# Performance work log

Measured on AMD Instinct MI355X. Metric: run time of the kernel, lower is better.

Reference implementation:

```python
import jax, jax.numpy as jnp
import numpy as np
from jax import lax

EPS = 1e-5

def conv2d(x, w, pad, dil):
    # x: NCHW, w: OIHW
    return lax.conv_general_dilated(
        x, w, window_strides=(1, 1), padding=[(pad, pad), (pad, pad)],
        rhs_dilation=(dil, dil), dimension_numbers=("NCHW", "OIHW", "NCHW"))

def batchnorm(x, gamma, beta):
    # training-mode BN: batch statistics over (N, H, W), biased variance
    m = x.mean(axis=(0, 2, 3), keepdims=True)
    v = x.var(axis=(0, 2, 3), keepdims=True)
    xh = (x - m) * lax.rsqrt(v + EPS)
    return gamma[None, :, None, None] * xh + beta[None, :, None, None]

def maxpool2(x):
    return lax.reduce_window(x, -jnp.inf, lax.max, (1, 1, 2, 2), (1, 1, 2, 2), "VALID")

def mhsa(x, wq, bq, wk, bk, wv, bv, rel_h, rel_w, heads=1):
    B, C, H, W = x.shape
    N = H * W
    d = C // heads
    q = (conv2d(x, wq, 0, 1) + bq[None, :, None, None]).reshape(B, heads, d, N)
    k = (conv2d(x, wk, 0, 1) + bk[None, :, None, None]).reshape(B, heads, d, N)
    v = (conv2d(x, wv, 0, 1) + bv[None, :, None, None]).reshape(B, heads, d, N)
    # content-content: q^T k -> [B, h, N, N]
    cc = jnp.einsum("bhdn,bhdm->bhnm", q, k)
    # content-position: (rel_h + rel_w) reshaped to [h, d, N], transposed, times q
    pos = (rel_h + rel_w).reshape(heads, d, N)  # broadcast-sum [1,h,d,1,H]+[1,h,d,W,1]
    cp = jnp.einsum("hnd,bhdm->bhnm", jnp.swapaxes(pos, 1, 2), q)
    attn = jax.nn.softmax(cc + cp, axis=-1)
    # out = v @ attn^T
    out = jnp.einsum("bhdn,bhmn->bhdm", v, attn)
    return out.reshape(B, C, H, W)


def setup_inputs() -> dict:
    key = jax.random.key(0)
    ks = jax.random.split(key, 16)
    B, in_ch, out_ch, S = 4, 128, 256, 64
    c4 = out_ch // 4  # 64 = MHSA channel dim
    w_scale = 0.05
    inp = {
        "x": jax.random.normal(ks[0], (B, in_ch, 2 * S, 2 * S), jnp.float32),
        "dc_w1": jax.random.normal(ks[1], (out_ch, in_ch, 3, 3), jnp.float32) * w_scale,
        "dc_b1": jnp.zeros((out_ch,), jnp.float32),
        "dc_g1": jnp.ones((out_ch,), jnp.float32),
        "dc_be1": jnp.zeros((out_ch,), jnp.float32),
        "dc_w2": jax.random.normal(ks[2], (out_ch, out_ch, 3, 3), jnp.float32) * w_scale,
        "dc_b2": jnp.zeros((out_ch,), jnp.float32),
        "dc_g2": jnp.ones((out_ch,), jnp.float32),
        "dc_be2": jnp.zeros((out_ch,), jnp.float32),
        "aspp1_w": jax.random.normal(ks[3], (c4, out_ch, 1, 1), jnp.float32) * w_scale,
        "aspp1_g": jnp.ones((c4,), jnp.float32),
        "aspp1_b": jnp.zeros((c4,), jnp.float32),
        "aspp2_w": jax.random.normal(ks[4], (c4, out_ch, 3, 3), jnp.float32) * w_scale,
        "aspp2_g": jnp.ones((c4,), jnp.float32),
        "aspp2_b": jnp.zeros((c4,), jnp.float32),
        "aspp3_w": jax.random.normal(ks[5], (c4, out_ch, 3, 3), jnp.float32) * w_scale,
        "aspp3_g": jnp.ones((c4,), jnp.float32),
        "aspp3_b": jnp.zeros((c4,), jnp.float32),
        "aspp4_w": jax.random.normal(ks[6], (c4, out_ch, 3, 3), jnp.float32) * w_scale,
        "aspp4_g": jnp.ones((c4,), jnp.float32),
        "aspp4_b": jnp.zeros((c4,), jnp.float32),
        "wq": jax.random.normal(ks[7], (c4, c4, 1, 1), jnp.float32) * w_scale,
        "bq": jnp.zeros((c4,), jnp.float32),
        "wk": jax.random.normal(ks[8], (c4, c4, 1, 1), jnp.float32) * w_scale,
        "bk": jnp.zeros((c4,), jnp.float32),
        "wv": jax.random.normal(ks[9], (c4, c4, 1, 1), jnp.float32) * w_scale,
        "bv": jnp.zeros((c4,), jnp.float32),
        "rel_h": jax.random.normal(ks[10], (1, 1, c4, 1, S), jnp.float32),
        "rel_w": jax.random.normal(ks[11], (1, 1, c4, S, 1), jnp.float32),
    }
    return inp


def reference(x, dc_w1, dc_b1, dc_g1, dc_be1, dc_w2, dc_b2, dc_g2, dc_be2,
              aspp1_w, aspp1_g, aspp1_b, aspp2_w, aspp2_g, aspp2_b,
              aspp3_w, aspp3_g, aspp3_b, aspp4_w, aspp4_g, aspp4_b,
              wq, bq, wk, bk, wv, bv, rel_h, rel_w):
    dilations = (1, 3, 6, 9)
    # mpconv: MaxPool2d(2) -> double_conv
    h = maxpool2(x)
    h = jax.nn.relu(batchnorm(conv2d(h, dc_w1, 1, 1) + dc_b1[None, :, None, None], dc_g1, dc_be1))
    h = jax.nn.relu(batchnorm(conv2d(h, dc_w2, 1, 1) + dc_b2[None, :, None, None], dc_g2, dc_be2))

    aspp = [(aspp1_w, aspp1_g, aspp1_b), (aspp2_w, aspp2_g, aspp2_b),
            (aspp3_w, aspp3_g, aspp3_b), (aspp4_w, aspp4_g, aspp4_b)]
    outs = []
    for (w, g, b), dil in zip(aspp, dilations):
        pad = 0 if dil == 1 else dil
        branch = jax.nn.relu(batchnorm(conv2d(h, w, pad, dil), g, b))
        outs.append(mhsa(branch, wq, bq, wk, bk, wv, bv, rel_h, rel_w))
    return jnp.concatenate(outs, axis=1)
```

## Files before the change

kernel.cpp:

```cpp
#include <hip/hip_runtime.h>
#include <math.h>

constexpr int Bn = 4;
constexpr int S  = 64;
constexpr int N  = 4096;

#define DEV static __device__ __forceinline__

typedef __attribute__((ext_vector_type(8))) short bf16x8;
typedef __attribute__((ext_vector_type(4))) float f32x4;

DEV unsigned short bfc(float x) {
  unsigned u = __float_as_uint(x);
  unsigned r = (u + 0x7FFFu + ((u >> 16) & 1u)) >> 16;
  return (unsigned short)r;
}

DEV void fma4(float4& a, float s, const float4 u) {
  a.x = fmaf(s, u.x, a.x); a.y = fmaf(s, u.y, a.y);
  a.z = fmaf(s, u.z, a.z); a.w = fmaf(s, u.w, a.w);
}

DEV void gload_lds16(const unsigned short* g, unsigned short* l) {
  __builtin_amdgcn_global_load_lds(
      (const __attribute__((address_space(1))) void*)g,
      (__attribute__((address_space(3))) void*)l, 16, 0, 0);
}

DEV unsigned cvtpk_bf16(float lo, float hi) {
  unsigned r;
  asm("v_cvt_pk_bf16_f32 %0, %1, %2" : "=v"(r) : "v"(lo), "v"(hi));
  return r;
}
DEV void pswap32(unsigned& a, unsigned& b) {
  asm("v_permlane32_swap_b32 %0, %1" : "+v"(a), "+v"(b));
}
DEV void pswap16(unsigned& a, unsigned& b) {
  asm("v_permlane16_swap_b32 %0, %1" : "+v"(a), "+v"(b));
}

__global__ __launch_bounds__(256) void wtr_all_kernel(
    const float* __restrict__ w1, const float* __restrict__ w2,
    const float* __restrict__ a0, const float* __restrict__ a1,
    const float* __restrict__ a2, const float* __restrict__ a3,
    unsigned short* __restrict__ wt1, unsigned short* __restrict__ wt2,
    unsigned short* __restrict__ wtbr) {
  const int blk = blockIdx.x;
  const float* src; unsigned short* dst; int Cin, Cout, T, base;
  if (blk < 1152)      { src = w1; dst = wt1; Cout = 256; Cin = 128; T = 9; base = 0; }
  else if (blk < 3456) { src = w2; dst = wt2; Cout = 256; Cin = 256; T = 9; base = 1152; }
  else if (blk < 3520) { src = a0; dst = wtbr + (size_t)4 * 64 * 256;
                         Cout = 64; Cin = 256; T = 1; base = 3456; }
  else if (blk < 4096) { src = a1; dst = wtbr + (size_t)1 * 9 * 64 * 256;
                         Cout = 64; Cin = 256; T = 9; base = 3520; }
  else if (blk < 4672) { src = a2; dst = wtbr + (size_t)2 * 9 * 64 * 256;
                         Cout = 64; Cin = 256; T = 9; base = 4096; }
  else                 { src = a3; dst = wtbr + (size_t)3 * 9 * 64 * 256;
                         Cout = 64; Cin = 256; T = 9; base = 4672; }
  int i = (blk - base) * 256 + threadIdx.x;
  int ci = i % Cin;
  int r  = i / Cin;
  int t  = r / Cout;
  int co = r - t * Cout;
  dst[i] = bfc(src[((size_t)co * Cin + ci) * T + t]);
}

__global__ __launch_bounds__(256) void pool_kernel(const float* __restrict__ x,
                                                   unsigned short* __restrict__ Pp1) {
  int i = blockIdx.x * 256 + threadIdx.x;
  int xg = i & 15, y = (i >> 4) & 63, c = (i >> 10) & 127, b = i >> 17;
  const float* s = x + (((size_t)(b * 128 + c) * 128) + 2 * y) * 128 + 8 * xg;
  float4 u0 = *(const float4*)(s), u1 = *(const float4*)(s + 4);
  float4 u2 = *(const float4*)(s + 128), u3 = *(const float4*)(s + 132);
  float m0 = fmaxf(fmaxf(u0.x, u0.y), fmaxf(u2.x, u2.y));
  float m1 = fmaxf(fmaxf(u0.z, u0.w), fmaxf(u2.z, u2.w));
  float m2 = fmaxf(fmaxf(u1.x, u1.y), fmaxf(u3.x, u3.y));
  float m3 = fmaxf(fmaxf(u1.z, u1.w), fmaxf(u3.z, u3.w));
  unsigned short* d = Pp1 + (((size_t)b * 66 + y + 1) * 66 + xg * 4 + 1) * 128 + c;
  d[0] = bfc(m0); d[128] = bfc(m1); d[256] = bfc(m2); d[384] = bfc(m3);
}

template <int CTOT>
__global__ __launch_bounds__(256) void dcconv_kernel(
    const unsigned short* __restrict__ in, const unsigned short* __restrict__ wt,
    float* __restrict__ out) {
  const int Wp = 66;
  const int w = threadIdx.x >> 6, lane = threadIdx.x & 63;
  const int ln = lane & 15, quad = lane >> 4;
  const int b = blockIdx.z, co0 = blockIdx.y * 32;
  const int n0 = blockIdx.x * 128 + w * 32;
  const unsigned short* inb = in + (size_t)b * Wp * Wp * CTOT;
  size_t pix[2];
#pragma unroll
  for (int j = 0; j < 2; j++) {
    int n = n0 + j * 16 + ln;
    int y = n >> 6, x = n & 63;
    pix[j] = ((size_t)y * Wp + x) * CTOT;
  }
  f32x4 acc[2][2];
#pragma unroll
  for (int i = 0; i < 2; i++)
#pragma unroll
    for (int j = 0; j < 2; j++) acc[i][j] = (f32x4)(0.f);
#pragma unroll
  for (int ky = 0; ky < 3; ky++)
#pragma unroll
    for (int kx = 0; kx < 3; kx++) {
      const size_t toff = ((size_t)ky * Wp + kx) * CTOT;
      const unsigned short* wtap = wt + (size_t)(ky * 3 + kx) * 256 * CTOT;
      for (int kc = 0; kc < CTOT / 32; kc++) {
        const int ko = kc * 32 + quad * 8;
        bf16x8 a[2], bb[2];
#pragma unroll
        for (int i = 0; i < 2; i++)
          a[i] = *(const bf16x8*)(wtap + (size_t)(co0 + i * 16 + ln) * CTOT + ko);
#pragma unroll
        for (int j = 0; j < 2; j++)
          bb[j] = *(const bf16x8*)(inb + pix[j] + toff + ko);
#pragma unroll
        for (int i = 0; i < 2; i++)
#pragma unroll
          for (int j = 0; j < 2; j++)
            acc[i][j] = __builtin_amdgcn_mfma_f32_16x16x32_bf16(a[i], bb[j], acc[i][j], 0, 0, 0);
      }
    }
#pragma unroll
  for (int i = 0; i < 2; i++)
#pragma unroll
    for (int j = 0; j < 2; j++)
#pragma unroll
      for (int r = 0; r < 4; r++)
        out[((size_t)(b * 256 + co0 + i * 16 + quad * 4 + r)) * N + n0 + j * 16 + ln] =
            acc[i][j][r];
}

__global__ __launch_bounds__(256) void branch_kernel(
    const unsigned short* __restrict__ in, const unsigned short* __restrict__ wtall,
    float* __restrict__ br) {
  const int Wp = 82, halo = 9, CIN = 256;
  const int w = threadIdx.x >> 6, lane = threadIdx.x & 63;
  const int ln = lane & 15, quad = lane >> 4;
  const int bb = blockIdx.y;
  const int kbr = bb >> 2, b = bb & 3;
  const int dil = (kbr == 0) ? 1 : 3 * kbr;
  const int klo = (kbr == 0) ? 1 : 0, khi = (kbr == 0) ? 2 : 3;
  const int hd = halo - dil;
  const int cw = (w & 1) * 32, nw = (w >> 1) * 32;
  const int n0 = blockIdx.x * 64 + nw;
  const unsigned short* inb = in + (size_t)b * Wp * Wp * CIN;
  size_t pix[2];
#pragma unroll
  for (int j = 0; j < 2; j++) {
    int n = n0 + j * 16 + ln;
    int y = n >> 6, x = n & 63;
    pix[j] = ((size_t)(y + hd) * Wp + x + hd) * CIN;
  }
  f32x4 acc[2][2];
#pragma unroll
  for (int i = 0; i < 2; i++)
#pragma unroll
    for (int j = 0; j < 2; j++) acc[i][j] = (f32x4)(0.f);
  for (int ky = klo; ky < khi; ky++)
    for (int kx = klo; kx < khi; kx++) {
      const size_t toff = ((size_t)ky * Wp + kx) * dil * CIN;
      const unsigned short* wtap =
          wtall + ((size_t)kbr * 9 + ky * 3 + kx) * 64 * CIN;
      for (int kc = 0; kc < CIN / 32; kc++) {
        const int ko = kc * 32 + quad * 8;
        bf16x8 a[2], bv[2];
#pragma unroll
        for (int i = 0; i < 2; i++)
          a[i] = *(const bf16x8*)(wtap + (size_t)(cw + i * 16 + ln) * CIN + ko);
#pragma unroll
        for (int j = 0; j < 2; j++)
          bv[j] = *(const bf16x8*)(inb + pix[j] + toff + ko);
#pragma unroll
        for (int i = 0; i < 2; i++)
#pragma unroll
          for (int j = 0; j < 2; j++)
            acc[i][j] = __builtin_amdgcn_mfma_f32_16x16x32_bf16(a[i], bv[j], acc[i][j], 0, 0, 0);
      }
    }
#pragma unroll
  for (int i = 0; i < 2; i++)
#pragma unroll
    for (int j = 0; j < 2; j++)
#pragma unroll
      for (int r = 0; r < 4; r++)
        br[((size_t)bb * 64 + cw + i * 16 + quad * 4 + r) * N + n0 + j * 16 + ln] =
            acc[i][j][r];
}

__global__ __launch_bounds__(256) void bn_stats_all_kernel(
    const float* __restrict__ br,
    const float* __restrict__ g0, const float* __restrict__ b0,
    const float* __restrict__ g1, const float* __restrict__ b1,
    const float* __restrict__ g2, const float* __restrict__ b2,
    const float* __restrict__ g3, const float* __restrict__ b3,
    float* __restrict__ sta) {
  const int kbr = blockIdx.x >> 6, c = blockIdx.x & 63;
  const float* gamma = kbr == 0 ? g0 : (kbr == 1 ? g1 : (kbr == 2 ? g2 : g3));
  const float* beta  = kbr == 0 ? b0 : (kbr == 1 ? b1 : (kbr == 2 ? b2 : b3));
  const float* t = br + (size_t)kbr * 1048576;
  float* ss = sta + kbr * 128;
  float s = 0.f, s2 = 0.f;
  for (int b = 0; b < Bn; b++) {
    const float* p = t + ((size_t)(b * 64 + c)) * N;
    for (int i = threadIdx.x; i < N / 4; i += 256) {
      float4 v = *(const float4*)(p + (size_t)i * 4);
      s += (v.x + v.y) + (v.z + v.w);
      s2 = fmaf(v.x, v.x, s2); s2 = fmaf(v.y, v.y, s2);
      s2 = fmaf(v.z, v.z, s2); s2 = fmaf(v.w, v.w, s2);
    }
  }
  for (int off = 32; off; off >>= 1) {
    s += __shfl_down(s, off, 64);
    s2 += __shfl_down(s2, off, 64);
  }
  __shared__ float rs[4], rs2[4];
  const int wid = threadIdx.x >> 6, lane = threadIdx.x & 63;
  if (lane == 0) { rs[wid] = s; rs2[wid] = s2; }
  __syncthreads();
  if (threadIdx.x == 0) {
    float S1 = rs[0] + rs[1] + rs[2] + rs[3];
    float S2 = rs2[0] + rs2[1] + rs2[2] + rs2[3];
    const float cnt = (float)(Bn * N);
    float mean = S1 / cnt;
    float var = S2 / cnt - mean * mean;
    float sc = gamma[c] * rsqrtf(var + 1e-5f);
    ss[2 * c] = sc;
    ss[2 * c + 1] = beta[c] - mean * sc;
  }
}

__global__ __launch_bounds__(256) void bn_stats_dc_kernel(
    const float* __restrict__ t, const float* __restrict__ gamma,
    const float* __restrict__ beta, float* __restrict__ ss) {
  const int c = blockIdx.x;
  float s = 0.f, s2 = 0.f;
  for (int b = 0; b < Bn; b++) {
    const float* p = t + ((size_t)(b * 256 + c)) * N;
    for (int i = threadIdx.x; i < N / 4; i += 256) {
      float4 v = *(const float4*)(p + (size_t)i * 4);
      s += (v.x + v.y) + (v.z + v.w);
      s2 = fmaf(v.x, v.x, s2); s2 = fmaf(v.y, v.y, s2);
      s2 = fmaf(v.z, v.z, s2); s2 = fmaf(v.w, v.w, s2);
    }
  }
  for (int off = 32; off; off >>= 1) {
    s += __shfl_down(s, off, 64);
    s2 += __shfl_down(s2, off, 64);
  }
  __shared__ float rs[4], rs2[4];
  const int wid = threadIdx.x >> 6, lane = threadIdx.x & 63;
  if (lane == 0) { rs[wid] = s; rs2[wid] = s2; }
  __syncthreads();
  if (threadIdx.x == 0) {
    float S1 = rs[0] + rs[1] + rs[2] + rs[3];
    float S2 = rs2[0] + rs2[1] + rs2[2] + rs2[3];
    const float cnt = (float)(Bn * N);
    float mean = S1 / cnt;
    float var = S2 / cnt - mean * mean;
    float sc = gamma[c] * rsqrtf(var + 1e-5f);
    ss[2 * c] = sc;
    ss[2 * c + 1] = beta[c] - mean * sc;
  }
}

__global__ __launch_bounds__(256) void bn_norm_pad_kernel(
    const float* __restrict__ ta, const float* __restrict__ ss,
    unsigned short* __restrict__ outp, int Wp, int halo) {
  int i = blockIdx.x * 256 + threadIdx.x;
  int n = i & 4095, cg = (i >> 12) & 63, b = i >> 18;
  int c0 = cg * 4;
  ushort4 pk;
  float v0, v1, v2, v3;
  {
    size_t i0 = ((size_t)(b * 256 + c0 + 0)) * N + n;
    size_t i1 = i0 + N, i2 = i1 + N, i3 = i2 + N;
    v0 = fmaxf(fmaf(ta[i0], ss[2 * (c0 + 0)], ss[2 * (c0 + 0) + 1]), 0.f);
    v1 = fmaxf(fmaf(ta[i1], ss[2 * (c0 + 1)], ss[2 * (c0 + 1) + 1]), 0.f);
    v2 = fmaxf(fmaf(ta[i2], ss[2 * (c0 + 2)], ss[2 * (c0 + 2) + 1]), 0.f);
    v3 = fmaxf(fmaf(ta[i3], ss[2 * (c0 + 3)], ss[2 * (c0 + 3) + 1]), 0.f);
  }
  pk.x = bfc(v0); pk.y = bfc(v1); pk.z = bfc(v2); pk.w = bfc(v3);
  int y = n >> 6, x = n & 63;
  *(ushort4*)(outp + (((size_t)b * Wp + y + halo) * Wp + x + halo) * 256 + c0) = pk;
}

__global__ __launch_bounds__(256) void qkv_kernel(
    const float* __restrict__ br, const float* __restrict__ sta,
    const float* __restrict__ wq, const float* __restrict__ bq,
    const float* __restrict__ wk, const float* __restrict__ bk,
    const float* __restrict__ wv, const float* __restrict__ bvb,
    unsigned short* __restrict__ qTo, unsigned short* __restrict__ kTo,
    unsigned short* __restrict__ vbo) {
  const int bb = blockIdx.z, dg = blockIdx.y;
  __shared__ float wl[3][64 * 16];
  __shared__ float ssl[128];
  const int d0b = dg * 16;
  if (threadIdx.x < 128) ssl[threadIdx.x] = sta[(bb >> 2) * 128 + threadIdx.x];
  for (int i = threadIdx.x; i < 64 * 16; i += 256) {
    const size_t widx = (size_t)(d0b + (i & 15)) * 64 + (i >> 4);
    wl[0][i] = wq[widx];
    wl[1][i] = wk[widx];
    wl[2][i] = wv[widx];
  }
  __syncthreads();
  const int tn = threadIdx.x & 63, td = threadIdx.x >> 6;
  const int n0 = blockIdx.x * 256 + tn * 4;
  const int d0 = d0b + td * 4;
  const float* inb = br + (size_t)bb * 64 * N;
  float4 acc[3][4];
#pragma unroll
  for (int j = 0; j < 4; j++) {
    float bq_ = bq[d0 + j], bk_ = bk[d0 + j], bv_ = bvb[d0 + j];
    acc[0][j] = make_float4(bq_, bq_, bq_, bq_);
    acc[1][j] = make_float4(bk_, bk_, bk_, bk_);
    acc[2][j] = make_float4(bv_, bv_, bv_, bv_);
  }
  for (int ci = 0; ci < 64; ci++) {
    float4 u = *(const float4*)(inb + (size_t)ci * N + n0);
    const float sc = ssl[2 * ci], of = ssl[2 * ci + 1];
    u.x = fmaxf(fmaf(u.x, sc, of), 0.f);
    u.y = fmaxf(fmaf(u.y, sc, of), 0.f);
    u.z = fmaxf(fmaf(u.z, sc, of), 0.f);
    u.w = fmaxf(fmaf(u.w, sc, of), 0.f);
#pragma unroll
    for (int p = 0; p < 3; p++) {
      float4 wv4 = *(const float4*)(&wl[p][ci * 16 + td * 4]);
      fma4(acc[p][0], wv4.x, u); fma4(acc[p][1], wv4.y, u);
      fma4(acc[p][2], wv4.z, u); fma4(acc[p][3], wv4.w, u);
    }
  }
  const size_t slab = (size_t)bb * N * 64;
#pragma unroll
  for (int p = 0; p < 2; p++) {
    unsigned short* o = (p == 0 ? qTo : kTo) + slab;
#pragma unroll
    for (int nn = 0; nn < 4; nn++) {
      ushort4 pk;
      pk.x = bfc(((const float*)&acc[p][0])[nn]);
      pk.y = bfc(((const float*)&acc[p][1])[nn]);
      pk.z = bfc(((const float*)&acc[p][2])[nn]);
      pk.w = bfc(((const float*)&acc[p][3])[nn]);
      *(ushort4*)(o + (size_t)(n0 + nn) * 64 + d0) = pk;
    }
  }
  {
    unsigned short* o = vbo + slab;
#pragma unroll
    for (int j = 0; j < 4; j++) {
      ushort4 pk;
      pk.x = bfc(acc[2][j].x); pk.y = bfc(acc[2][j].y);
      pk.z = bfc(acc[2][j].z); pk.w = bfc(acc[2][j].w);
      *(ushort4*)(o + (size_t)(d0 + j) * N + n0) = pk;
    }
  }
}

__global__ __launch_bounds__(256) void posT_kernel(
    const float* __restrict__ rel_h, const float* __restrict__ rel_w,
    unsigned short* __restrict__ posT) {
  int i = blockIdx.x * 256 + threadIdx.x;
  int n = i >> 4, dq = (i & 15) * 4;
  int h = n >> 6, wc = n & 63;
  ushort4 pk;
  pk.x = bfc(rel_w[(dq + 0) * 64 + h] + rel_h[(dq + 0) * 64 + wc]);
  pk.y = bfc(rel_w[(dq + 1) * 64 + h] + rel_h[(dq + 1) * 64 + wc]);
  pk.z = bfc(rel_w[(dq + 2) * 64 + h] + rel_h[(dq + 2) * 64 + wc]);
  pk.w = bfc(rel_w[(dq + 3) * 64 + h] + rel_h[(dq + 3) * 64 + wc]);
  *(ushort4*)(posT + (size_t)n * 64 + dq) = pk;
}

__global__ __launch_bounds__(256, 3) void flash3_kernel(
    const unsigned short* __restrict__ qT, const unsigned short* __restrict__ kT,
    const unsigned short* __restrict__ posT, const unsigned short* __restrict__ vb,
    float* __restrict__ o_part, float* __restrict__ ml) {
  const int lin = blockIdx.x;
  const int xcd = lin & 7, slot = lin >> 3;
  const int bb = xcd * 2 + (slot & 1);
  const int rest = slot >> 1;
  const int mtile = rest & 31, split = rest >> 5;
  const size_t slab = (size_t)bb * N * 64;
  const unsigned short* qTs = qT + slab;
  const unsigned short* kTs = kT + slab;
  const unsigned short* vbs = vb + slab;
  const int w = threadIdx.x >> 6, lane = threadIdx.x & 63;
  const int ln = lane & 15, quad = lane >> 4;
  const int m0 = mtile * 128 + w * 32;
  __shared__ __align__(16) unsigned short As[2][4][64][32];

  const unsigned short* ssrc = (w < 2) ? kTs : qTs;
  const int rsub = lane >> 2;
  const int csw  = (lane & 3) ^ ((lane >> 3) & 3);
  const int ksub = (w & 1) * 32 + csw * 8;
  auto stage = [&](int c0, int bufi) {
#pragma unroll
    for (int j = 0; j < 4; j++)
      gload_lds16(ssrc + (size_t)(c0 + j * 16 + rsub) * 64 + ksub,
                  &As[bufi][w][j * 16][0]);
  };

  bf16x8 bq[4][2];
#pragma unroll
  for (int s = 0; s < 4; s++) {
    const unsigned short* src = (s < 2) ? qTs : posT;
#pragma unroll
    for (int mf = 0; mf < 2; mf++)
      bq[s][mf] = *(const bf16x8*)(src + (size_t)(m0 + mf * 16 + ln) * 64 +
                                   (s & 1) * 32 + quad * 8);
  }

  float m_run[2] = {-3.0e38f, -3.0e38f}, l_run[2] = {0.f, 0.f};
  f32x4 o_acc[4][2];
#pragma unroll
  for (int dt = 0; dt < 4; dt++)
#pragma unroll
    for (int mf = 0; mf < 2; mf++) o_acc[dt][mf] = (f32x4)(0.f);

  const int qsw = (quad ^ ((ln >> 1) & 3)) * 8;
  const int cbeg = split * 1024;
  stage(cbeg, 0);
  for (int t = 0; t < 16; t++) {
    const int c0 = cbeg + t * 64;
    const int buf = t & 1;
    __syncthreads();
    if (t < 15) stage(c0 + 64, buf ^ 1);
    f32x4 st[4][2];
#pragma unroll
    for (int jt = 0; jt < 4; jt++)
#pragma unroll
      for (int mf = 0; mf < 2; mf++) st[jt][mf] = (f32x4)(0.f);
    __builtin_amdgcn_s_setprio(1);
#pragma unroll
    for (int s = 0; s < 4; s++) {
#pragma unroll
      for (int jt = 0; jt < 4; jt++) {
        bf16x8 a = *(const bf16x8*)(&As[buf][s][jt * 16 + ln][qsw]);
#pragma unroll
        for (int mf = 0; mf < 2; mf++)
          st[jt][mf] = __builtin_amdgcn_mfma_f32_16x16x32_bf16(a, bq[s][mf], st[jt][mf], 0, 0, 0);
      }
    }
    __builtin_amdgcn_s_setprio(0);
    bf16x8 av[2][4];
#pragma unroll
    for (int tt = 0; tt < 2; tt++)
#pragma unroll
      for (int dt = 0; dt < 4; dt++)
        av[tt][dt] = *(const bf16x8*)(vbs + (size_t)(dt * 16 + ln) * N + c0 + tt * 32 + quad * 8);
    unsigned P0[2][4], P1[2][4];
#pragma unroll
    for (int mf = 0; mf < 2; mf++) {
      float mj[4];
#pragma unroll
      for (int jt = 0; jt < 4; jt++)
        mj[jt] = fmaxf(fmaxf(st[jt][mf][0], st[jt][mf][1]),
                       fmaxf(st[jt][mf][2], st[jt][mf][3]));
      float mx = fmaxf(fmaxf(mj[0], mj[1]), fmaxf(mj[2], mj[3]));
      mx = fmaxf(mx, __shfl_xor(mx, 16, 64));
      mx = fmaxf(mx, __shfl_xor(mx, 32, 64));
      if (!__all(mx <= m_run[mf])) {
        const float m_new = fmaxf(m_run[mf], mx);
        const float alpha = __expf(m_run[mf] - m_new);
        l_run[mf] *= alpha;
#pragma unroll
        for (int dt = 0; dt < 4; dt++)
#pragma unroll
          for (int r = 0; r < 4; r++) o_acc[dt][mf][r] *= alpha;
        m_run[mf] = m_new;
      }
      const float mc = m_run[mf];
      float psum = 0.f;
#pragma unroll
      for (int jt = 0; jt < 4; jt++) {
        float e0 = __expf(st[jt][mf][0] - mc);
        float e1 = __expf(st[jt][mf][1] - mc);
        float e2 = __expf(st[jt][mf][2] - mc);
        float e3 = __expf(st[jt][mf][3] - mc);
        psum += (e0 + e1) + (e2 + e3);
        P0[mf][jt] = cvtpk_bf16(e0, e1);
        P1[mf][jt] = cvtpk_bf16(e2, e3);
      }
      psum += __shfl_xor(psum, 16, 64);
      psum += __shfl_xor(psum, 32, 64);
      l_run[mf] += psum;
    }
    __builtin_amdgcn_s_setprio(1);
#pragma unroll
    for (int tt = 0; tt < 2; tt++) {
#pragma unroll
      for (int mf = 0; mf < 2; mf++) {
        unsigned x0 = P0[mf][2 * tt], y0 = P0[mf][2 * tt + 1];
        pswap32(x0, y0); pswap16(x0, y0);
        unsigned x1 = P1[mf][2 * tt], y1 = P1[mf][2 * tt + 1];
        pswap32(x1, y1); pswap16(x1, y1);
        union { unsigned u[4]; bf16x8 v; } bp;
        bp.u[0] = x0; bp.u[1] = x1; bp.u[2] = y0; bp.u[3] = y1;
#pragma unroll
        for (int dt = 0; dt < 4; dt++)
          o_acc[dt][mf] = __builtin_amdgcn_mfma_f32_16x16x32_bf16(av[tt][dt], bp.v, o_acc[dt][mf], 0, 0, 0);
      }
    }
    __builtin_amdgcn_s_setprio(0);
  }
  float* ob = o_part + ((size_t)(split * 16 + bb) * 64) * N;
#pragma unroll
  for (int dt = 0; dt < 4; dt++)
#pragma unroll
    for (int mf = 0; mf < 2; mf++)
#pragma unroll
      for (int r = 0; r < 4; r++) {
        int d = dt * 16 + quad * 4 + r;
        ob[(size_t)d * N + m0 + mf * 16 + ln] = o_acc[dt][mf][r];
      }
  if (quad == 0) {
#pragma unroll
    for (int mf = 0; mf < 2; mf++) {
      int m = m0 + mf * 16 + ln;
      ml[((size_t)(split * 16 + bb) * 2 + 0) * N + m] = m_run[mf];
      ml[((size_t)(split * 16 + bb) * 2 + 1) * N + m] = l_run[mf];
    }
  }
}

__global__ __launch_bounds__(256) void comb_kernel(const float* __restrict__ o_part,
                                                   const float* __restrict__ ml,
                                                   float* __restrict__ out) {
  int i = blockIdx.x * 256 + threadIdx.x;
  int m4 = i & 1023, d = (i >> 10) & 63, bb = i >> 16;
  int kbr = bb >> 2, b = bb & 3;
  float mvv[4][4], lvv[4][4];
#pragma unroll
  for (int s = 0; s < 4; s++) {
    float4 t0 = *(const float4*)(ml + ((size_t)(s * 16 + bb) * 2 + 0) * N + m4 * 4);
    float4 t1 = *(const float4*)(ml + ((size_t)(s * 16 + bb) * 2 + 1) * N + m4 * 4);
    mvv[s][0] = t0.x; mvv[s][1] = t0.y; mvv[s][2] = t0.z; mvv[s][3] = t0.w;
    lvv[s][0] = t1.x; lvv[s][1] = t1.y; lvv[s][2] = t1.z; lvv[s][3] = t1.w;
  }
  float w4[4][4];
#pragma unroll
  for (int mm = 0; mm < 4; mm++) {
    float M = fmaxf(fmaxf(mvv[0][mm], mvv[1][mm]), fmaxf(mvv[2][mm], mvv[3][mm]));
    float wsc[4], denom = 0.f;
#pragma unroll
    for (int s = 0; s < 4; s++) {
      wsc[s] = __expf(mvv[s][mm] - M);
      denom = fmaf(wsc[s], lvv[s][mm], denom);
    }
    float inv = 1.0f / denom;
#pragma unroll
    for (int s = 0; s < 4; s++) w4[s][mm] = wsc[s] * inv;
  }
  float4 acc = make_float4(0.f, 0.f, 0.f, 0.f);
#pragma unroll
  for (int s = 0; s < 4; s++) {
    const float4 o = *(const float4*)(o_part + ((size_t)(s * 16 + bb) * 64 + d) * N + m4 * 4);
    acc.x = fmaf(o.x, w4[s][0], acc.x); acc.y = fmaf(o.y, w4[s][1], acc.y);
    acc.z = fmaf(o.z, w4[s][2], acc.z); acc.w = fmaf(o.w, w4[s][3], acc.w);
  }
  *(float4*)(out + ((size_t)(b * 256 + kbr * 64 + d)) * N + m4 * 4) = acc;
}

extern "C" void kernel_launch(void* const* d_in, const int* in_sizes, int n_in,
                              void* d_out, int out_size, void* d_ws, size_t ws_size,
                              hipStream_t stream) {
  const float* x      = (const float*)d_in[0];
  const float* dc_w1  = (const float*)d_in[1];
  const float* dc_g1  = (const float*)d_in[3];
  const float* dc_be1 = (const float*)d_in[4];
  const float* dc_w2  = (const float*)d_in[5];
  const float* dc_g2  = (const float*)d_in[7];
  const float* dc_be2 = (const float*)d_in[8];
  const float* aspp_w[4] = {(const float*)d_in[9],  (const float*)d_in[12],
                            (const float*)d_in[15], (const float*)d_in[18]};
  const float* aspp_g[4] = {(const float*)d_in[10], (const float*)d_in[13],
                            (const float*)d_in[16], (const float*)d_in[19]};
  const float* aspp_b[4] = {(const float*)d_in[11], (const float*)d_in[14],
                            (const float*)d_in[17], (const float*)d_in[20]};
  const float* wq = (const float*)d_in[21];
  const float* bq = (const float*)d_in[22];
  const float* wk = (const float*)d_in[23];
  const float* bk = (const float*)d_in[24];
  const float* wv = (const float*)d_in[25];
  const float* bv = (const float*)d_in[26];
  const float* rel_h = (const float*)d_in[27];
  const float* rel_w = (const float*)d_in[28];
  float* out = (float*)d_out;

  float* ws = (float*)d_ws;
  size_t off = 0;
  auto alloc = [&](size_t nf) { float* p = ws + off; off += nf; return p; };
  unsigned short* Pp1 = (unsigned short*)alloc((size_t)4 * 66 * 66 * 128 / 2 + 64);
  unsigned short* Pp2 = (unsigned short*)alloc((size_t)4 * 66 * 66 * 256 / 2 + 64);
  unsigned short* Pp3 = (unsigned short*)alloc((size_t)4 * 82 * 82 * 256 / 2 + 64);
  const size_t HALF = (size_t)4 * 256 * N;
  float* t1   = alloc(HALF);
  float* br   = alloc((size_t)4 * 4 * 64 * N);
  float* st1  = alloc(512);
  float* st2  = alloc(512);
  float* sta  = alloc(512);
  unsigned short* qT    = (unsigned short*)alloc((size_t)16 * N * 64 / 2);
  unsigned short* kT    = (unsigned short*)alloc((size_t)16 * N * 64 / 2);
  unsigned short* vb    = (unsigned short*)alloc((size_t)16 * N * 64 / 2);
  unsigned short* posT  = (unsigned short*)alloc((size_t)N * 64 / 2);
  unsigned short* wt1   = (unsigned short*)alloc((size_t)9 * 256 * 128 / 2);
  unsigned short* wt2   = (unsigned short*)alloc((size_t)9 * 256 * 256 / 2);
  unsigned short* wtbr  = (unsigned short*)alloc((size_t)4 * 9 * 64 * 256 / 2);
  float* o_part = alloc((size_t)4 * 16 * 64 * N);
  float* mlb    = alloc((size_t)4 * 16 * 2 * N);

  hipMemsetAsync(Pp1, 0, (size_t)4 * 66 * 66 * 128 * 2, stream);
  hipMemsetAsync(Pp2, 0, (size_t)4 * 66 * 66 * 256 * 2, stream);
  hipMemsetAsync(Pp3, 0, (size_t)4 * 82 * 82 * 256 * 2, stream);
  hipMemsetAsync(wtbr, 0, (size_t)4 * 9 * 64 * 256 * 2, stream);

  wtr_all_kernel<<<5248, 256, 0, stream>>>(dc_w1, dc_w2, aspp_w[0], aspp_w[1],
                                           aspp_w[2], aspp_w[3], wt1, wt2, wtbr);

  pool_kernel<<<2048, 256, 0, stream>>>(x, Pp1);

  dcconv_kernel<128><<<dim3(32, 8, 4), 256, 0, stream>>>(Pp1, wt1, t1);
  bn_stats_dc_kernel<<<256, 256, 0, stream>>>(t1, dc_g1, dc_be1, st1);
  bn_norm_pad_kernel<<<4096, 256, 0, stream>>>(t1, st1, Pp2, 66, 1);
  dcconv_kernel<256><<<dim3(32, 8, 4), 256, 0, stream>>>(Pp2, wt2, t1);
  bn_stats_dc_kernel<<<256, 256, 0, stream>>>(t1, dc_g2, dc_be2, st2);
  bn_norm_pad_kernel<<<4096, 256, 0, stream>>>(t1, st2, Pp3, 82, 9);

  branch_kernel<<<dim3(64, 16), 256, 0, stream>>>(Pp3, wtbr, br);
  bn_stats_all_kernel<<<256, 256, 0, stream>>>(
      br, aspp_g[0], aspp_b[0], aspp_g[1], aspp_b[1],
      aspp_g[2], aspp_b[2], aspp_g[3], aspp_b[3], sta);

  qkv_kernel<<<dim3(16, 4, 16), 256, 0, stream>>>(br, sta, wq, bq, wk, bk,
                                                  wv, bv, qT, kT, vb);
  posT_kernel<<<256, 256, 0, stream>>>(rel_h, rel_w, posT);

  flash3_kernel<<<dim3(2048), 256, 0, stream>>>(qT, kT, posT, vb, o_part, mlb);
  comb_kernel<<<4096, 256, 0, stream>>>(o_part, mlb, out);
}
```

Measured before the change: 693.3 us.

## Split double-conv reduction over input channels and widen output-channel tile

The double-conv kernel now computes 64 output channels per block instead of 32, which improves reuse of input loads. It also splits the input-channel reduction into two halves written to separate fp32 buffers, keeping the same block count. The downstream BN stats and normalize kernels read both partial buffers and sum them. This adds a second full-size intermediate buffer and extra memory traffic in the BN kernels, in exchange for more MFMA work per input load.

```diff
diff --git a/kernel.cpp b/kernel.cpp
--- a/kernel.cpp
+++ b/kernel.cpp
@@ -84,12 +84,14 @@
 __global__ __launch_bounds__(256) void dcconv_kernel(
     const unsigned short* __restrict__ in, const unsigned short* __restrict__ wt,
     float* __restrict__ out) {
-  const int Wp = 66;
+  const int Wp = 66, CSEG = CTOT / 2;
   const int w = threadIdx.x >> 6, lane = threadIdx.x & 63;
   const int ln = lane & 15, quad = lane >> 4;
-  const int b = blockIdx.z, co0 = blockIdx.y * 32;
+  const int b = blockIdx.z >> 1, h = blockIdx.z & 1, co0 = blockIdx.y * 64;
   const int n0 = blockIdx.x * 128 + w * 32;
-  const unsigned short* inb = in + (size_t)b * Wp * Wp * CTOT;
+  const unsigned short* inb = in + (size_t)b * Wp * Wp * CTOT + h * CSEG;
+  const unsigned short* wth = wt + h * CSEG;
+  float* outh = out + (size_t)h * 4 * 256 * N;
   size_t pix[2];
 #pragma unroll
   for (int j = 0; j < 2; j++) {
@@ -97,9 +99,9 @@
     int y = n >> 6, x = n & 63;
     pix[j] = ((size_t)y * Wp + x) * CTOT;
   }
-  f32x4 acc[2][2];
-#pragma unroll
-  for (int i = 0; i < 2; i++)
+  f32x4 acc[4][2];
+#pragma unroll
+  for (int i = 0; i < 4; i++)
 #pragma unroll
     for (int j = 0; j < 2; j++) acc[i][j] = (f32x4)(0.f);
 #pragma unroll
@@ -107,30 +109,30 @@
 #pragma unroll
     for (int kx = 0; kx < 3; kx++) {
       const size_t toff = ((size_t)ky * Wp + kx) * CTOT;
-      const unsigned short* wtap = wt + (size_t)(ky * 3 + kx) * 256 * CTOT;
-      for (int kc = 0; kc < CTOT / 32; kc++) {
+      const unsigned short* wtap = wth + (size_t)(ky * 3 + kx) * 256 * CTOT;
+      for (int kc = 0; kc < CSEG / 32; kc++) {
         const int ko = kc * 32 + quad * 8;
-        bf16x8 a[2], bb[2];
-#pragma unroll
-        for (int i = 0; i < 2; i++)
+        bf16x8 a[4], bb[2];
+#pragma unroll
+        for (int i = 0; i < 4; i++)
           a[i] = *(const bf16x8*)(wtap + (size_t)(co0 + i * 16 + ln) * CTOT + ko);
 #pragma unroll
         for (int j = 0; j < 2; j++)
           bb[j] = *(const bf16x8*)(inb + pix[j] + toff + ko);
 #pragma unroll
-        for (int i = 0; i < 2; i++)
+        for (int i = 0; i < 4; i++)
 #pragma unroll
           for (int j = 0; j < 2; j++)
             acc[i][j] = __builtin_amdgcn_mfma_f32_16x16x32_bf16(a[i], bb[j], acc[i][j], 0, 0, 0);
       }
     }
 #pragma unroll
-  for (int i = 0; i < 2; i++)
+  for (int i = 0; i < 4; i++)
 #pragma unroll
     for (int j = 0; j < 2; j++)
 #pragma unroll
       for (int r = 0; r < 4; r++)
-        out[((size_t)(b * 256 + co0 + i * 16 + quad * 4 + r)) * N + n0 + j * 16 + ln] =
+        outh[((size_t)(b * 256 + co0 + i * 16 + quad * 4 + r)) * N + n0 + j * 16 + ln] =
             acc[i][j][r];
 }
 
@@ -233,18 +235,22 @@
   }
 }
 
-__global__ __launch_bounds__(256) void bn_stats_dc_kernel(
-    const float* __restrict__ t, const float* __restrict__ gamma,
-    const float* __restrict__ beta, float* __restrict__ ss) {
+__global__ __launch_bounds__(256) void bn_stats2_kernel(
+    const float* __restrict__ ta, const float* __restrict__ tb,
+    const float* __restrict__ gamma, const float* __restrict__ beta,
+    float* __restrict__ ss, int C) {
   const int c = blockIdx.x;
   float s = 0.f, s2 = 0.f;
   for (int b = 0; b < Bn; b++) {
-    const float* p = t + ((size_t)(b * 256 + c)) * N;
+    const size_t base = ((size_t)(b * C + c)) * N;
     for (int i = threadIdx.x; i < N / 4; i += 256) {
-      float4 v = *(const float4*)(p + (size_t)i * 4);
-      s += (v.x + v.y) + (v.z + v.w);
-      s2 = fmaf(v.x, v.x, s2); s2 = fmaf(v.y, v.y, s2);
-      s2 = fmaf(v.z, v.z, s2); s2 = fmaf(v.w, v.w, s2);
+      float4 va = *(const float4*)(ta + base + (size_t)i * 4);
+      float4 vb = *(const float4*)(tb + base + (size_t)i * 4);
+      float v0 = va.x + vb.x, v1 = va.y + vb.y;
+      float v2 = va.z + vb.z, v3 = va.w + vb.w;
+      s += (v0 + v1) + (v2 + v3);
+      s2 = fmaf(v0, v0, s2); s2 = fmaf(v1, v1, s2);
+      s2 = fmaf(v2, v2, s2); s2 = fmaf(v3, v3, s2);
     }
   }
   for (int off = 32; off; off >>= 1) {
@@ -267,9 +273,10 @@
   }
 }
 
-__global__ __launch_bounds__(256) void bn_norm_pad_kernel(
-    const float* __restrict__ ta, const float* __restrict__ ss,
-    unsigned short* __restrict__ outp, int Wp, int halo) {
+__global__ __launch_bounds__(256) void bn_norm_pad2_kernel(
+    const float* __restrict__ ta, const float* __restrict__ tb,
+    const float* __restrict__ ss, unsigned short* __restrict__ outp,
+    int Wp, int halo) {
   int i = blockIdx.x * 256 + threadIdx.x;
   int n = i & 4095, cg = (i >> 12) & 63, b = i >> 18;
   int c0 = cg * 4;
@@ -278,10 +285,10 @@
   {
     size_t i0 = ((size_t)(b * 256 + c0 + 0)) * N + n;
     size_t i1 = i0 + N, i2 = i1 + N, i3 = i2 + N;
-    v0 = fmaxf(fmaf(ta[i0], ss[2 * (c0 + 0)], ss[2 * (c0 + 0) + 1]), 0.f);
-    v1 = fmaxf(fmaf(ta[i1], ss[2 * (c0 + 1)], ss[2 * (c0 + 1) + 1]), 0.f);
-    v2 = fmaxf(fmaf(ta[i2], ss[2 * (c0 + 2)], ss[2 * (c0 + 2) + 1]), 0.f);
-    v3 = fmaxf(fmaf(ta[i3], ss[2 * (c0 + 3)], ss[2 * (c0 + 3) + 1]), 0.f);
+    v0 = fmaxf(fmaf(ta[i0] + tb[i0], ss[2 * (c0 + 0)], ss[2 * (c0 + 0) + 1]), 0.f);
+    v1 = fmaxf(fmaf(ta[i1] + tb[i1], ss[2 * (c0 + 1)], ss[2 * (c0 + 1) + 1]), 0.f);
+    v2 = fmaxf(fmaf(ta[i2] + tb[i2], ss[2 * (c0 + 2)], ss[2 * (c0 + 2) + 1]), 0.f);
+    v3 = fmaxf(fmaf(ta[i3] + tb[i3], ss[2 * (c0 + 3)], ss[2 * (c0 + 3) + 1]), 0.f);
   }
   pk.x = bfc(v0); pk.y = bfc(v1); pk.z = bfc(v2); pk.w = bfc(v3);
   int y = n >> 6, x = n & 63;
@@ -596,7 +603,7 @@
   unsigned short* Pp2 = (unsigned short*)alloc((size_t)4 * 66 * 66 * 256 / 2 + 64);
   unsigned short* Pp3 = (unsigned short*)alloc((size_t)4 * 82 * 82 * 256 / 2 + 64);
   const size_t HALF = (size_t)4 * 256 * N;
-  float* t1   = alloc(HALF);
+  float* t1   = alloc(2 * HALF);
   float* br   = alloc((size_t)4 * 4 * 64 * N);
   float* st1  = alloc(512);
   float* st2  = alloc(512);
@@ -621,12 +628,12 @@
 
   pool_kernel<<<2048, 256, 0, stream>>>(x, Pp1);
 
-  dcconv_kernel<128><<<dim3(32, 8, 4), 256, 0, stream>>>(Pp1, wt1, t1);
-  bn_stats_dc_kernel<<<256, 256, 0, stream>>>(t1, dc_g1, dc_be1, st1);
-  bn_norm_pad_kernel<<<4096, 256, 0, stream>>>(t1, st1, Pp2, 66, 1);
-  dcconv_kernel<256><<<dim3(32, 8, 4), 256, 0, stream>>>(Pp2, wt2, t1);
-  bn_stats_dc_kernel<<<256, 256, 0, stream>>>(t1, dc_g2, dc_be2, st2);
-  bn_norm_pad_kernel<<<4096, 256, 0, stream>>>(t1, st2, Pp3, 82, 9);
+  dcconv_kernel<128><<<dim3(32, 4, 8), 256, 0, stream>>>(Pp1, wt1, t1);
+  bn_stats2_kernel<<<256, 256, 0, stream>>>(t1, t1 + HALF, dc_g1, dc_be1, st1, 256);
+  bn_norm_pad2_kernel<<<4096, 256, 0, stream>>>(t1, t1 + HALF, st1, Pp2, 66, 1);
+  dcconv_kernel<256><<<dim3(32, 4, 8), 256, 0, stream>>>(Pp2, wt2, t1);
+  bn_stats2_kernel<<<256, 256, 0, stream>>>(t1, t1 + HALF, dc_g2, dc_be2, st2, 256);
+  bn_norm_pad2_kernel<<<4096, 256, 0, stream>>>(t1, t1 + HALF, st2, Pp3, 82, 9);
 
   branch_kernel<<<dim3(64, 16), 256, 0, stream>>>(Pp3, wtbr, br);
   bn_stats_all_kernel<<<256, 256, 0, stream>>>(
```

Result: faster. 654.7 us (-5.6%).
